# Kernel tuning notes

Measured on AMD Instinct MI355X. Metric: run time of the kernel, lower is better.

Reference implementation:

```python
import jax, jax.numpy as jnp
import numpy as np
from jax import lax
from functools import partial

TAU = 2.0
V_TH = 1.0
ATAN_ALPHA = 2.0
BN_EPS = 1e-5

# Heaviside spike with ATan surrogate gradient (spikingjelly surrogate.ATan, alpha=2)
@jax.custom_vjp
def atan_spike(x):
    return (x >= 0).astype(x.dtype)

def _atan_fwd(x):
    return atan_spike(x), x

def _atan_bwd(x, g):
    # d/dx ~ alpha/2 / (1 + (pi/2 * alpha * x)^2)
    s = (jnp.pi / 2.0) * ATAN_ALPHA * x
    return (g * (ATAN_ALPHA / 2.0) / (1.0 + s * s),)

atan_spike.defvjp(_atan_fwd, _atan_bwd)

def lif_multistep(x_seq):
    # x_seq: [T, B, ...]; LIFNode: decay_input=True, v_reset=0 (hard reset), v0=0
    def step(v, x):
        v = v + (x - v) / TAU           # charge with input decay
        s = atan_spike(v - V_TH)        # fire
        v = v * (1.0 - s)               # hard reset to 0 (reset not detached)
        return v, s
    v0 = jnp.zeros_like(x_seq[0])
    _, s_seq = lax.scan(step, v0, x_seq)
    return s_seq

def conv2d_seq(x_seq, w):
    # x_seq: [T, B, C, H, W] -> flatten T into batch for the conv
    T, B, C, H, W = x_seq.shape
    x = x_seq.reshape(T * B, C, H, W)
    y = lax.conv_general_dilated(x, w, window_strides=(1, 1),
                                 padding=[(1, 1), (1, 1)],
                                 dimension_numbers=('NCHW', 'OIHW', 'NCHW'))
    return y.reshape(T, B, w.shape[0], H, W)

def batchnorm_seq(x_seq, gamma, beta):
    # training-mode BN: stats over merged (T*B, H, W) per channel
    mean = jnp.mean(x_seq, axis=(0, 1, 3, 4), keepdims=True)
    var = jnp.var(x_seq, axis=(0, 1, 3, 4), keepdims=True)
    xhat = (x_seq - mean) * lax.rsqrt(var + BN_EPS)
    return xhat * gamma[None, None, :, None, None] + beta[None, None, :, None, None]

def avgpool2_seq(x_seq):
    T, B, C, H, W = x_seq.shape
    x = x_seq.reshape(T * B, C, H, W)
    y = lax.reduce_window(x, 0.0, lax.add, (1, 1, 2, 2), (1, 1, 2, 2), 'VALID') * 0.25
    return y.reshape(T, B, C, H // 2, W // 2)


def setup_inputs() -> dict:
    key = jax.random.key(0)
    ks = jax.random.split(key, 6)
    T, B = 8, 128
    return {
        'x_seq': jax.random.uniform(ks[0], (T, B, 3, 32, 32), jnp.float32),
        'conv1_w': jax.random.normal(ks[1], (64, 3, 3, 3), jnp.float32) * (1.0 / np.sqrt(3 * 9)),
        'bn1_g': jnp.ones((64,), jnp.float32),
        'bn1_b': jnp.zeros((64,), jnp.float32),
        'conv2_w': jax.random.normal(ks[2], (128, 64, 3, 3), jnp.float32) * (1.0 / np.sqrt(64 * 9)),
        'bn2_g': jnp.ones((128,), jnp.float32),
        'bn2_b': jnp.zeros((128,), jnp.float32),
        'fc1_w': jax.random.normal(ks[3], (256, 8192), jnp.float32) * (1.0 / np.sqrt(8192)),
        'fc2_w': jax.random.normal(ks[4], (10, 256), jnp.float32) * (1.0 / np.sqrt(256)),
        'fc2_b': jnp.zeros((10,), jnp.float32),
    }


def reference(x_seq, conv1_w, bn1_g, bn1_b, conv2_w, bn2_g, bn2_b, fc1_w, fc2_w, fc2_b):
    x = avgpool2_seq(lif_multistep(batchnorm_seq(conv2d_seq(x_seq, conv1_w), bn1_g, bn1_b)))
    x = avgpool2_seq(lif_multistep(batchnorm_seq(conv2d_seq(x, conv2_w), bn2_g, bn2_b)))
    T, B = x.shape[0], x.shape[1]
    x = x.reshape(T, B, -1)                                  # [T, B, 8192]
    x = lif_multistep(jnp.einsum('tbi,oi->tbo', x, fc1_w))   # [T, B, 256]
    logits_seq = jnp.einsum('tbi,oi->tbo', x, fc2_w) + fc2_b # [T, B, 10]
    return logits_seq
```

## Files before the change

kernel.cpp:

```cpp
#include <hip/hip_runtime.h>


#define LIF_STEP(vv, xx, ss) do { \
    vv = fmaf((xx) - vv, 0.5f, vv); \
    ss = (vv >= 1.0f) ? 1.0f : 0.0f; \
    vv = (vv >= 1.0f) ? 0.0f : vv; \
  } while (0)

typedef __attribute__((ext_vector_type(8))) short short8;
typedef __attribute__((ext_vector_type(4))) float f32x4;

__device__ __forceinline__ float bf2f(unsigned short u) {
  return __uint_as_float(((unsigned)u) << 16);
}
__device__ __forceinline__ unsigned short f2bf(float f) {
  return (unsigned short)(__float_as_uint(f) >> 16);
}

#define OFF_POOL1   0u
#define OFF_POOL2   8388608u
#define OFF_PRE     12582912u
#define OFF_STATS   46137344u
#define OFF_FC1S    46162304u
#define OFF_A2      46424448u
#define OFF_B1      46535040u
#define OFF_A1      49680768u
#define ZERO_STATS 24576u

__global__ __launch_bounds__(256) void zero_kernel(float* __restrict__ p, unsigned n) {
  unsigned i = blockIdx.x * 256u + threadIdx.x;
  if (i < n) p[i] = 0.0f;
}

__global__ __launch_bounds__(256) void prep_w1(const float* __restrict__ w, unsigned short* __restrict__ A1) {
  int i = blockIdx.x * 256 + threadIdx.x;
  if (i >= 2048) return;
  int co = i >> 5, k = i & 31;
  float wv = 0.f;
  if (k < 27) {
    int tap = k / 3, ci = k - tap * 3;
    wv = w[co * 27 + ci * 9 + tap];
  }
  unsigned short hi = f2bf(wv);
  float rem = wv - bf2f(hi);
  unsigned short lo = f2bf(rem);
  float rem2 = rem - bf2f(lo);
  A1[i] = hi;
  A1[2048 + i] = lo;
  A1[4096 + i] = f2bf(rem2);
}

__global__ __launch_bounds__(256) void prep_w2(const float* __restrict__ w, unsigned short* __restrict__ A2) {
  int i = blockIdx.x * 256 + threadIdx.x;
  if (i >= 73728) return;
  int co = i / 576, r = i - co * 576;
  int ci = r / 9, t9 = r - ci * 9;
  int k = t9 * 64 + ci;
  int kc = k >> 5, q = (k >> 3) & 3, j = k & 7;
  int off = ((kc * 128 + co) * 4 + q) * 8 + j;
  float wv = w[i];
  unsigned short hi = f2bf(wv);
  float rem = wv - bf2f(hi);
  unsigned short lo = f2bf(rem);
  float rem2 = rem - bf2f(lo);
  A2[off] = hi;
  A2[73728 + off] = lo;
  A2[147456 + off] = f2bf(rem2);
}

__global__ __launch_bounds__(256) void prep_b1(const float* __restrict__ w, unsigned short* __restrict__ B1) {
  __shared__ unsigned short sh[2][8192];
  int blk = blockIdx.x;
  int sv = blk >> 7, opair = blk & 127;
  int tid = threadIdx.x;
  for (int o_l = 0; o_l < 2; ++o_l) {
    for (int it = 0; it < 32; ++it) {
      int korig = tid + 256 * it;
      float wv = w[(size_t)(opair * 2 + o_l) * 8192 + korig];
      unsigned short hi = f2bf(wv);
      float rem = wv - bf2f(hi);
      unsigned short lo = f2bf(rem);
      unsigned short pc = (sv == 0) ? hi : (sv == 1) ? lo : f2bf(rem - bf2f(lo));
      int k = (korig & 63) * 128 + (korig >> 6);
      sh[o_l][k] = pc;
    }
  }
  __syncthreads();
  unsigned short* outp = B1 + (size_t)sv * 2097152;
  for (int it = 0; it < 64; ++it) {
    int idx = tid + 256 * it;
    int kc = idx >> 6, r = idx & 63;
    int o_l = r >> 5, m = r & 31;
    outp[kc * 8192 + opair * 64 + r] = sh[o_l][kc * 32 + m];
  }
}

__global__ void finalize_bn1(const float* __restrict__ s1p,
                             const float* __restrict__ g, const float* __restrict__ b,
                             float* __restrict__ scale, float* __restrict__ shift, float inv_n) {
  int c = threadIdx.x;
  float s1 = 0.f, s2 = 0.f;
#pragma unroll 8
  for (int sp = 0; sp < 64; ++sp) {
    s1 += s1p[sp * 128 + c];
    s2 += s1p[sp * 128 + 64 + c];
  }
  float mean = s1 * inv_n;
  float var = fmaxf(s2 * inv_n - mean * mean, 0.0f);
  float rstd = rsqrtf(var + 1e-5f);
  float sc = g[c] * rstd;
  scale[c] = sc;
  shift[c] = fmaf(-mean, sc, b[c]);
}

__global__ void finalize_bn2(const float* __restrict__ s2p,
                             const float* __restrict__ g, const float* __restrict__ b,
                             float* __restrict__ scale, float* __restrict__ shift, float inv_n) {
  int c = threadIdx.x;
  float s1 = 0.f, s2 = 0.f;
#pragma unroll 8
  for (int sp = 0; sp < 64; ++sp) {
    s1 += s2p[sp * 256 + c];
    s2 += s2p[sp * 256 + 128 + c];
  }
  float mean = s1 * inv_n;
  float var = fmaxf(s2 * inv_n - mean * mean, 0.0f);
  float rstd = rsqrtf(var + 1e-5f);
  float sc = g[c] * rstd;
  scale[c] = sc;
  shift[c] = fmaf(-mean, sc, b[c]);
}

__global__ __launch_bounds__(256) void conv1_pass1_mfma(const float* __restrict__ x,
    const unsigned short* __restrict__ A1, float* __restrict__ s1p) {
  int b = blockIdx.x >> 3, yq = blockIdx.x & 7;
  int y0 = yq * 4;
  int sp = blockIdx.x & 63;
  int tid = threadIdx.x, wave = tid >> 6, lane = tid & 63;
  int xl = lane & 15, q = lane >> 4;
  __shared__ float xs[648];
  short8 A[3][4];
#pragma unroll
  for (int mt = 0; mt < 4; ++mt) {
    int aoff = (mt * 16 + xl) * 32 + q * 8;
    A[0][mt] = *(const short8*)(A1 + aoff);
    A[1][mt] = *(const short8*)(A1 + 2048 + aoff);
    A[2][mt] = *(const short8*)(A1 + 4096 + aoff);
  }
  int cb[8]; bool vld[8];
#pragma unroll
  for (int j = 0; j < 8; ++j) {
    int k = q * 8 + j;
    int tap = k / 3, ci = k - tap * 3;
    int dy = tap / 3, dx = tap - dy * 3;
    vld[j] = (k < 27);
    cb[j] = ci * 216 + (wave + dy) * 36 + dx + xl;
  }
  float s1[4][4], s2[4][4];
#pragma unroll
  for (int mt = 0; mt < 4; ++mt)
#pragma unroll
    for (int reg = 0; reg < 4; ++reg) { s1[mt][reg] = 0.f; s2[mt][reg] = 0.f; }

#pragma unroll 1
  for (int t = 0; t < 8; ++t) {
    int tb = t * 128 + b;
    const float* xb = x + tb * 3072;
    __syncthreads();
    for (int i = tid; i < 648; i += 256) {
      int ci = i / 216, r1 = i - ci * 216;
      int rr = r1 / 36, c = r1 - rr * 36;
      int gy = y0 - 1 + rr, gx = c - 1;
      xs[i] = ((unsigned)gy < 32u && (unsigned)gx < 32u) ? xb[(ci * 32 + gy) * 32 + gx] : 0.f;
    }
    __syncthreads();
    f32x4 acc[2][4];
#pragma unroll
    for (int tile = 0; tile < 2; ++tile)
#pragma unroll
      for (int mt = 0; mt < 4; ++mt) acc[tile][mt] = (f32x4){0.f, 0.f, 0.f, 0.f};
#pragma unroll
    for (int tile = 0; tile < 2; ++tile) {
      short8 Bh = (short8){0,0,0,0,0,0,0,0};
      short8 Bl = (short8){0,0,0,0,0,0,0,0};
      short8 Bll = (short8){0,0,0,0,0,0,0,0};
#pragma unroll
      for (int j = 0; j < 8; ++j) {
        float xv = vld[j] ? xs[cb[j] + tile * 16] : 0.f;
        unsigned short h = f2bf(xv);
        float r = xv - bf2f(h);
        unsigned short l = f2bf(r);
        float r2 = r - bf2f(l);
        Bh[j] = (short)h; Bl[j] = (short)l; Bll[j] = (short)f2bf(r2);
      }
#pragma unroll
      for (int mt = 0; mt < 4; ++mt) {
        f32x4 a = acc[tile][mt];
        a = __builtin_amdgcn_mfma_f32_16x16x32_bf16(A[0][mt], Bh, a, 0, 0, 0);
        a = __builtin_amdgcn_mfma_f32_16x16x32_bf16(A[1][mt], Bh, a, 0, 0, 0);
        a = __builtin_amdgcn_mfma_f32_16x16x32_bf16(A[2][mt], Bh, a, 0, 0, 0);
        a = __builtin_amdgcn_mfma_f32_16x16x32_bf16(A[0][mt], Bl, a, 0, 0, 0);
        a = __builtin_amdgcn_mfma_f32_16x16x32_bf16(A[1][mt], Bl, a, 0, 0, 0);
        a = __builtin_amdgcn_mfma_f32_16x16x32_bf16(A[2][mt], Bl, a, 0, 0, 0);
        a = __builtin_amdgcn_mfma_f32_16x16x32_bf16(A[0][mt], Bll, a, 0, 0, 0);
        a = __builtin_amdgcn_mfma_f32_16x16x32_bf16(A[1][mt], Bll, a, 0, 0, 0);
        acc[tile][mt] = a;
      }
    }
#pragma unroll
    for (int tile = 0; tile < 2; ++tile)
#pragma unroll
      for (int mt = 0; mt < 4; ++mt)
#pragma unroll
        for (int reg = 0; reg < 4; ++reg) {
          float val = acc[tile][mt][reg];
          s1[mt][reg] += val; s2[mt][reg] = fmaf(val, val, s2[mt][reg]);
        }
  }
#pragma unroll
  for (int mt = 0; mt < 4; ++mt)
#pragma unroll
    for (int reg = 0; reg < 4; ++reg) {
      float a1 = s1[mt][reg], a2 = s2[mt][reg];
#pragma unroll
      for (int off = 1; off < 16; off <<= 1) { a1 += __shfl_xor(a1, off); a2 += __shfl_xor(a2, off); }
      if (xl == 0) {
        int co = mt * 16 + q * 4 + reg;
        atomicAdd(&s1p[sp * 128 + co], a1);
        atomicAdd(&s1p[sp * 128 + 64 + co], a2);
      }
    }
}

__global__ __launch_bounds__(256) void conv1_fused_mfma(const float* __restrict__ x,
    const unsigned short* __restrict__ A1, const float* __restrict__ scale,
    const float* __restrict__ shift, unsigned short* __restrict__ pool1) {
  int b = blockIdx.x >> 3, yq = blockIdx.x & 7;
  int y0 = yq * 4;
  int tid = threadIdx.x, wave = tid >> 6, lane = tid & 63;
  int xl = lane & 15, q = lane >> 4;
  __shared__ float xs[648];
  __shared__ unsigned short shout[4 * 16 * 72];
  short8 A[3][4];
#pragma unroll
  for (int mt = 0; mt < 4; ++mt) {
    int aoff = (mt * 16 + xl) * 32 + q * 8;
    A[0][mt] = *(const short8*)(A1 + aoff);
    A[1][mt] = *(const short8*)(A1 + 2048 + aoff);
    A[2][mt] = *(const short8*)(A1 + 4096 + aoff);
  }
  int cb[8]; bool vld[8];
#pragma unroll
  for (int j = 0; j < 8; ++j) {
    int k = q * 8 + j;
    int tap = k / 3, ci = k - tap * 3;
    int dy = tap / 3, dx = tap - dy * 3;
    vld[j] = (k < 27);
    cb[j] = ci * 216 + (wave + dy) * 36 + dx + xl;
  }
  float scr[4][4], shr[4][4];
#pragma unroll
  for (int mt = 0; mt < 4; ++mt)
#pragma unroll
    for (int reg = 0; reg < 4; ++reg) {
      int co = mt * 16 + q * 4 + reg;
      scr[mt][reg] = scale[co]; shr[mt][reg] = shift[co];
    }
  float v[2][4][4];
#pragma unroll
  for (int tile = 0; tile < 2; ++tile)
#pragma unroll
    for (int mt = 0; mt < 4; ++mt)
#pragma unroll
      for (int reg = 0; reg < 4; ++reg) v[tile][mt][reg] = 0.f;

#pragma unroll 1
  for (int t = 0; t < 8; ++t) {
    int tb = t * 128 + b;
    const float* xb = x + tb * 3072;
    __syncthreads();
    for (int i = tid; i < 648; i += 256) {
      int ci = i / 216, r1 = i - ci * 216;
      int rr = r1 / 36, c = r1 - rr * 36;
      int gy = y0 - 1 + rr, gx = c - 1;
      xs[i] = ((unsigned)gy < 32u && (unsigned)gx < 32u) ? xb[(ci * 32 + gy) * 32 + gx] : 0.f;
    }
    __syncthreads();
    f32x4 acc[2][4];
#pragma unroll
    for (int tile = 0; tile < 2; ++tile)
#pragma unroll
      for (int mt = 0; mt < 4; ++mt) acc[tile][mt] = (f32x4){0.f, 0.f, 0.f, 0.f};
#pragma unroll
    for (int tile = 0; tile < 2; ++tile) {
      short8 Bh = (short8){0,0,0,0,0,0,0,0};
      short8 Bl = (short8){0,0,0,0,0,0,0,0};
      short8 Bll = (short8){0,0,0,0,0,0,0,0};
#pragma unroll
      for (int j = 0; j < 8; ++j) {
        float xv = vld[j] ? xs[cb[j] + tile * 16] : 0.f;
        unsigned short h = f2bf(xv);
        float r = xv - bf2f(h);
        unsigned short l = f2bf(r);
        float r2 = r - bf2f(l);
        Bh[j] = (short)h; Bl[j] = (short)l; Bll[j] = (short)f2bf(r2);
      }
#pragma unroll
      for (int mt = 0; mt < 4; ++mt) {
        f32x4 a = acc[tile][mt];
        a = __builtin_amdgcn_mfma_f32_16x16x32_bf16(A[0][mt], Bh, a, 0, 0, 0);
        a = __builtin_amdgcn_mfma_f32_16x16x32_bf16(A[1][mt], Bh, a, 0, 0, 0);
        a = __builtin_amdgcn_mfma_f32_16x16x32_bf16(A[2][mt], Bh, a, 0, 0, 0);
        a = __builtin_amdgcn_mfma_f32_16x16x32_bf16(A[0][mt], Bl, a, 0, 0, 0);
        a = __builtin_amdgcn_mfma_f32_16x16x32_bf16(A[1][mt], Bl, a, 0, 0, 0);
        a = __builtin_amdgcn_mfma_f32_16x16x32_bf16(A[2][mt], Bl, a, 0, 0, 0);
        a = __builtin_amdgcn_mfma_f32_16x16x32_bf16(A[0][mt], Bll, a, 0, 0, 0);
        a = __builtin_amdgcn_mfma_f32_16x16x32_bf16(A[1][mt], Bll, a, 0, 0, 0);
        acc[tile][mt] = a;
      }
    }
#pragma unroll
    for (int mt = 0; mt < 4; ++mt)
#pragma unroll
      for (int rp = 0; rp < 2; ++rp) {
        float hp[2][2];
#pragma unroll
        for (int tile = 0; tile < 2; ++tile)
#pragma unroll
          for (int e = 0; e < 2; ++e) {
            int reg = rp * 2 + e;
            float xv = fmaf(acc[tile][mt][reg], scr[mt][reg], shr[mt][reg]);
            float spk;
            LIF_STEP(v[tile][mt][reg], xv, spk);
            hp[tile][e] = spk + __shfl_xor(spk, 1);
          }
        int tw = xl & 1;
        float h0 = tw ? hp[1][0] : hp[0][0];
        float h1 = tw ? hp[1][1] : hp[0][1];
        unsigned u = (unsigned)f2bf(h0) | ((unsigned)f2bf(h1) << 16);
        int pp = tw * 8 + (xl >> 1);
        *(unsigned*)&shout[(wave * 16 + pp) * 72 + mt * 16 + q * 4 + rp * 2] = u;
      }
    __syncthreads();
    {
      int cg = tid >> 5, py_l = (tid >> 4) & 1, px = tid & 15;
      uint4 ua = *(const uint4*)&shout[((2 * py_l) * 16 + px) * 72 + cg * 8];
      uint4 ub = *(const uint4*)&shout[((2 * py_l + 1) * 16 + px) * 72 + cg * 8];
      const unsigned* pa = (const unsigned*)&ua;
      const unsigned* pb = (const unsigned*)&ub;
      unsigned o[4];
#pragma unroll
      for (int e = 0; e < 4; ++e) {
        float a0 = bf2f((unsigned short)(pa[e] & 0xffffu)), a1 = bf2f((unsigned short)(pa[e] >> 16));
        float b0 = bf2f((unsigned short)(pb[e] & 0xffffu)), b1 = bf2f((unsigned short)(pb[e] >> 16));
        o[e] = (unsigned)f2bf(0.25f * (a0 + b0)) | ((unsigned)f2bf(0.25f * (a1 + b1)) << 16);
      }
      int py = yq * 2 + py_l;
      *(uint4*)(pool1 + (size_t)tb * 16384 + cg * 2048 + (py * 16 + px) * 8) =
          make_uint4(o[0], o[1], o[2], o[3]);
    }
  }
}

__device__ __forceinline__ void c2_load_a(const unsigned short* __restrict__ A2, int kc,
                                          int m0, int xl, int q, short8 (&a)[2][3]) {
#pragma unroll
  for (int mt = 0; mt < 2; ++mt) {
    int aoff = ((kc * 128 + m0 + mt * 16 + xl) * 4 + q) * 8;
    a[mt][0] = *(const short8*)(A2 + aoff);
    a[mt][1] = *(const short8*)(A2 + 73728 + aoff);
    a[mt][2] = *(const short8*)(A2 + 147456 + aoff);
  }
}
__device__ __forceinline__ void c2_step(const unsigned short* __restrict__ simg, int kc,
                                        int xl, int q, short8 (&a)[2][3], f32x4 (&acc)[2][4]) {
  int tap = kc >> 1;
  int dy = tap / 3, dx = tap - dy * 3;
  int cgq = (kc & 1) * 4 + q;
#pragma unroll
  for (int yl = 0; yl < 4; ++yl) {
    int baddr = (((yl + dy) * 8 + cgq) * 18 + (xl + dx)) * 8;
    short8 bb = *(const short8*)(simg + baddr);
#pragma unroll
    for (int mt = 0; mt < 2; ++mt) {
      acc[mt][yl] = __builtin_amdgcn_mfma_f32_16x16x32_bf16(a[mt][0], bb, acc[mt][yl], 0, 0, 0);
      acc[mt][yl] = __builtin_amdgcn_mfma_f32_16x16x32_bf16(a[mt][1], bb, acc[mt][yl], 0, 0, 0);
      acc[mt][yl] = __builtin_amdgcn_mfma_f32_16x16x32_bf16(a[mt][2], bb, acc[mt][yl], 0, 0, 0);
    }
  }
}

__global__ __launch_bounds__(256, 2) void conv2_store_mfma(const unsigned short* __restrict__ pool1,
    const unsigned short* __restrict__ A2, float* __restrict__ preact, float* __restrict__ s2p) {
  int bx = blockIdx.x;
  int tb = bx >> 2, q4 = bx & 3;
  int sp = bx & 63;
  __shared__ unsigned short simg[6 * 8 * 18 * 8];
  int tid = threadIdx.x;
  const unsigned* src = (const unsigned*)(pool1 + (size_t)tb * 16384);
  unsigned* dstw = (unsigned*)simg;
  for (int i = tid; i < 3456; i += 256) {
    int cp = i & 3, rest = i >> 2;
    int jj = rest / 18, xx = rest - jj * 18;
    int cg = jj & 7, row_l = jj >> 3;
    int yi = q4 * 4 - 1 + row_l, gx = xx - 1;
    unsigned val = 0u;
    if ((unsigned)yi < 16u && (unsigned)gx < 16u)
      val = src[cg * 1024 + yi * 64 + gx * 4 + cp];
    dstw[i] = val;
  }
  __syncthreads();

  int wave = tid >> 6, lane = tid & 63;
  int xl = lane & 15, q = lane >> 4;
  int m0 = wave * 32;
  f32x4 acc[2][4];
#pragma unroll
  for (int mt = 0; mt < 2; ++mt)
#pragma unroll
    for (int yl = 0; yl < 4; ++yl) acc[mt][yl] = (f32x4){0.f, 0.f, 0.f, 0.f};

  short8 aA[2][3], aB[2][3];
  c2_load_a(A2, 0, m0, xl, q, aA);
#pragma unroll 1
  for (int kc = 0; kc < 18; kc += 2) {
    c2_load_a(A2, kc + 1, m0, xl, q, aB);
    c2_step(simg, kc, xl, q, aA, acc);
    if (kc + 2 < 18) c2_load_a(A2, kc + 2, m0, xl, q, aA);
    c2_step(simg, kc + 1, xl, q, aB, acc);
  }

  float* pre = preact + (size_t)tb * 32768;
#pragma unroll
  for (int mt = 0; mt < 2; ++mt)
#pragma unroll
    for (int reg = 0; reg < 4; ++reg) {
      int co = m0 + mt * 16 + q * 4 + reg;
      float s1 = 0.f, s2 = 0.f;
#pragma unroll
      for (int yl = 0; yl < 4; ++yl) {
        float val = acc[mt][yl][reg];
        int row = q4 * 4 + yl;
        pre[(row * 128 + co) * 16 + xl] = val;
        s1 += val; s2 = fmaf(val, val, s2);
      }
#pragma unroll
      for (int off = 1; off < 16; off <<= 1) {
        s1 += __shfl_xor(s1, off); s2 += __shfl_xor(s2, off);
      }
      if (xl == 0) {
        atomicAdd(&s2p[sp * 256 + co], s1);
        atomicAdd(&s2p[sp * 256 + 128 + co], s2);
      }
    }
}

__global__ __launch_bounds__(256) void bn2_lif_pool(const float* __restrict__ pre,
    const float* __restrict__ scale, const float* __restrict__ shift,
    unsigned short* __restrict__ pool2) {
  int b = blockIdx.x >> 3, py = blockIdx.x & 7;
  int tid = threadIdx.x;
  int co = tid >> 1, half = tid & 1;
  __shared__ unsigned short shout[8 * 136];
  float sc = scale[co], sh = shift[co];
  float v[4][4];
#pragma unroll
  for (int p = 0; p < 4; ++p)
#pragma unroll
    for (int e = 0; e < 4; ++e) v[p][e] = 0.f;

#pragma unroll 1
  for (int t = 0; t < 8; ++t) {
    const float* base = pre + ((size_t)((t * 128 + b) * 16 + 2 * py)) * 2048 + co * 16 + half * 8;
    __syncthreads();
    float4 r0a = *(const float4*)(base);
    float4 r0b = *(const float4*)(base + 4);
    float4 r1a = *(const float4*)(base + 2048);
    float4 r1b = *(const float4*)(base + 2048 + 4);
    float p00[4] = {r0a.x, r0a.z, r0b.x, r0b.z};
    float p01[4] = {r0a.y, r0a.w, r0b.y, r0b.w};
    float p10[4] = {r1a.x, r1a.z, r1b.x, r1b.z};
    float p11[4] = {r1a.y, r1a.w, r1b.y, r1b.w};
#pragma unroll
    for (int p = 0; p < 4; ++p) {
      float s00, s01, s10, s11, xv;
      xv = fmaf(p00[p], sc, sh); LIF_STEP(v[p][0], xv, s00);
      xv = fmaf(p01[p], sc, sh); LIF_STEP(v[p][1], xv, s01);
      xv = fmaf(p10[p], sc, sh); LIF_STEP(v[p][2], xv, s10);
      xv = fmaf(p11[p], sc, sh); LIF_STEP(v[p][3], xv, s11);
      shout[(half * 4 + p) * 136 + co] = f2bf(0.25f * (s00 + s01 + s10 + s11));
    }
    __syncthreads();
    {
      int s_l = tid >> 5, ci4 = (tid & 31) * 4;
      uint2 vv = *(const uint2*)&shout[s_l * 136 + ci4];
      *(uint2*)(pool2 + ((size_t)(t * 128 + b) * 64 + py * 8 + s_l) * 128 + ci4) = vv;
    }
  }
}

__global__ __launch_bounds__(256, 2) void fc1_mfma(const unsigned short* __restrict__ pool2,
    const unsigned short* __restrict__ B1, float* __restrict__ partial) {
  int bx = blockIdx.x;
  int t_o = bx & 1, tbt = (bx >> 1) & 15, kb = bx >> 5;
  int tid = threadIdx.x, wave = tid >> 6, lane = tid & 63;
  int xl = lane & 15, q = lane >> 4;
  int m0 = t_o * 128 + wave * 32;
  int n0 = tbt * 64;
  __shared__ unsigned short sB[64 * 42];
  f32x4 acc[2][4];
#pragma unroll
  for (int mt = 0; mt < 2; ++mt)
#pragma unroll
    for (int nt = 0; nt < 4; ++nt) acc[mt][nt] = (f32x4){0.f, 0.f, 0.f, 0.f};

#pragma unroll 1
  for (int kc0 = 0; kc0 < 16; ++kc0) {
    int kc = kb * 16 + kc0;
    __syncthreads();
    {
      int tb_l = tid >> 2, kq = tid & 3;
      uint4 vv = *(const uint4*)(pool2 + (size_t)(n0 + tb_l) * 8192 + kc * 32 + kq * 8);
      *(uint4*)(sB + tb_l * 42 + kq * 8) = vv;
    }
    __syncthreads();
    short8 a[2][3];
#pragma unroll
    for (int mt = 0; mt < 2; ++mt) {
      int aoff = ((kc * 256 + m0 + mt * 16 + xl) * 4 + q) * 8;
      a[mt][0] = *(const short8*)(B1 + aoff);
      a[mt][1] = *(const short8*)(B1 + 2097152 + aoff);
      a[mt][2] = *(const short8*)(B1 + 4194304 + aoff);
    }
#pragma unroll
    for (int nt = 0; nt < 4; ++nt) {
      short8 bb = *(const short8*)(sB + (nt * 16 + xl) * 42 + q * 8);
#pragma unroll
      for (int mt = 0; mt < 2; ++mt) {
        acc[mt][nt] = __builtin_amdgcn_mfma_f32_16x16x32_bf16(a[mt][0], bb, acc[mt][nt], 0, 0, 0);
        acc[mt][nt] = __builtin_amdgcn_mfma_f32_16x16x32_bf16(a[mt][1], bb, acc[mt][nt], 0, 0, 0);
        acc[mt][nt] = __builtin_amdgcn_mfma_f32_16x16x32_bf16(a[mt][2], bb, acc[mt][nt], 0, 0, 0);
      }
    }
  }
#pragma unroll
  for (int mt = 0; mt < 2; ++mt)
#pragma unroll
    for (int nt = 0; nt < 4; ++nt)
#pragma unroll
      for (int reg = 0; reg < 4; ++reg) {
        int o = m0 + mt * 16 + q * 4 + reg;
        partial[((size_t)kb * 256 + o) * 1024 + n0 + nt * 16 + xl] = acc[mt][nt][reg];
      }
}

__global__ __launch_bounds__(256) void reduce_lif(const float* __restrict__ partial, float* __restrict__ fs) {
  int idx = blockIdx.x * 256 + threadIdx.x;
  int o = idx >> 7, b = idx & 127;
  float v = 0.f;
#pragma unroll 1
  for (int t = 0; t < 8; ++t) {
    float xv = 0.f;
#pragma unroll
    for (int kb = 0; kb < 16; ++kb)
      xv += partial[((size_t)kb * 256 + o) * 1024 + t * 128 + b];
    float s;
    LIF_STEP(v, xv, s);
    fs[t * 32768 + b * 256 + o] = s;
  }
}

__global__ __launch_bounds__(256) void fc2_kernel(const float* __restrict__ fs, const float* __restrict__ w,
                                                  const float* __restrict__ bias, float* __restrict__ outp) {
  int tb = blockIdx.x;
  __shared__ float sv[256];
  int tid = threadIdx.x;
  sv[tid] = fs[tb * 256 + tid];
  __syncthreads();
  if (tid < 10) {
    float a = bias[tid];
    const float* wr = w + tid * 256;
#pragma unroll 8
    for (int o = 0; o < 256; ++o) a = fmaf(sv[o], wr[o], a);
    outp[tb * 10 + tid] = a;
  }
}

extern "C" void kernel_launch(void* const* d_in, const int* in_sizes, int n_in,
                              void* d_out, int out_size, void* d_ws, size_t ws_size,
                              hipStream_t stream) {
  (void)in_sizes; (void)n_in; (void)out_size; (void)ws_size;
  const float* x_seq   = (const float*)d_in[0];
  const float* conv1_w = (const float*)d_in[1];
  const float* bn1_g   = (const float*)d_in[2];
  const float* bn1_b   = (const float*)d_in[3];
  const float* conv2_w = (const float*)d_in[4];
  const float* bn2_g   = (const float*)d_in[5];
  const float* bn2_b   = (const float*)d_in[6];
  const float* fc1_w   = (const float*)d_in[7];
  const float* fc2_w   = (const float*)d_in[8];
  const float* fc2_b   = (const float*)d_in[9];
  float* out = (float*)d_out;
  float* ws  = (float*)d_ws;

  unsigned short* pool1 = (unsigned short*)(ws + OFF_POOL1);
  float* fc1_part = ws + OFF_POOL1;
  unsigned short* pool2 = (unsigned short*)(ws + OFF_POOL2);
  float* preact  = ws + OFF_PRE;
  float* fc1_s   = ws + OFF_FC1S;
  unsigned short* A2 = (unsigned short*)(ws + OFF_A2);
  unsigned short* B1 = (unsigned short*)(ws + OFF_B1);
  unsigned short* A1 = (unsigned short*)(ws + OFF_A1);
  float* st      = ws + OFF_STATS;
  float* s1p    = st;
  float* s2p    = st + 8192;
  float* bn1_sc = st + 24576;  float* bn1_sh = st + 24640;
  float* bn2_sc = st + 24704;  float* bn2_sh = st + 24832;

  zero_kernel<<<96, 256, 0, stream>>>(st, ZERO_STATS);
  prep_w1<<<8, 256, 0, stream>>>(conv1_w, A1);
  prep_w2<<<288, 256, 0, stream>>>(conv2_w, A2);
  prep_b1<<<384, 256, 0, stream>>>(fc1_w, B1);
  conv1_pass1_mfma<<<1024, 256, 0, stream>>>(x_seq, A1, s1p);
  finalize_bn1<<<1, 64, 0, stream>>>(s1p, bn1_g, bn1_b, bn1_sc, bn1_sh, 1.0f / 1048576.0f);
  conv1_fused_mfma<<<1024, 256, 0, stream>>>(x_seq, A1, bn1_sc, bn1_sh, pool1);
  conv2_store_mfma<<<4096, 256, 0, stream>>>(pool1, A2, preact, s2p);
  finalize_bn2<<<1, 128, 0, stream>>>(s2p, bn2_g, bn2_b, bn2_sc, bn2_sh, 1.0f / 262144.0f);
  bn2_lif_pool<<<1024, 256, 0, stream>>>(preact, bn2_sc, bn2_sh, pool2);
  fc1_mfma<<<512, 256, 0, stream>>>(pool2, B1, fc1_part);
  reduce_lif<<<128, 256, 0, stream>>>(fc1_part, fc1_s);
  fc2_kernel<<<1024, 256, 0, stream>>>(fc1_s, fc2_w, fc2_b, out);
}
```

Before: 402.5 us.

## Enlarge conv2 spatial tile to 8 rows and halve fc1 barrier count

Each conv2 block now computes 8 output rows instead of 4, so each loaded A2 weight fragment feeds twice as many MFMAs and the halo overhead in shared memory drops. The grid is halved to 2048 blocks and the accumulators double to 64 floats per lane, which adds register pressure under the 2-blocks-per-SM launch bound. Separately, fc1 stages two K-chunks per barrier pair into a double-sized shared buffer, halving the number of __syncthreads.

```diff
diff --git a/kernel.cpp b/kernel.cpp
--- a/kernel.cpp
+++ b/kernel.cpp
@@ -372,13 +372,13 @@
     a[mt][2] = *(const short8*)(A2 + 147456 + aoff);
   }
 }
-__device__ __forceinline__ void c2_step(const unsigned short* __restrict__ simg, int kc,
-                                        int xl, int q, short8 (&a)[2][3], f32x4 (&acc)[2][4]) {
+__device__ __forceinline__ void c2_step8(const unsigned short* __restrict__ simg, int kc,
+                                         int xl, int q, short8 (&a)[2][3], f32x4 (&acc)[2][8]) {
   int tap = kc >> 1;
   int dy = tap / 3, dx = tap - dy * 3;
   int cgq = (kc & 1) * 4 + q;
 #pragma unroll
-  for (int yl = 0; yl < 4; ++yl) {
+  for (int yl = 0; yl < 8; ++yl) {
     int baddr = (((yl + dy) * 8 + cgq) * 18 + (xl + dx)) * 8;
     short8 bb = *(const short8*)(simg + baddr);
 #pragma unroll
@@ -393,17 +393,17 @@
 __global__ __launch_bounds__(256, 2) void conv2_store_mfma(const unsigned short* __restrict__ pool1,
     const unsigned short* __restrict__ A2, float* __restrict__ preact, float* __restrict__ s2p) {
   int bx = blockIdx.x;
-  int tb = bx >> 2, q4 = bx & 3;
+  int tb = bx >> 1, half = bx & 1;
   int sp = bx & 63;
-  __shared__ unsigned short simg[6 * 8 * 18 * 8];
+  __shared__ unsigned short simg[10 * 8 * 18 * 8];
   int tid = threadIdx.x;
   const unsigned* src = (const unsigned*)(pool1 + (size_t)tb * 16384);
   unsigned* dstw = (unsigned*)simg;
-  for (int i = tid; i < 3456; i += 256) {
+  for (int i = tid; i < 5760; i += 256) {
     int cp = i & 3, rest = i >> 2;
     int jj = rest / 18, xx = rest - jj * 18;
     int cg = jj & 7, row_l = jj >> 3;
-    int yi = q4 * 4 - 1 + row_l, gx = xx - 1;
+    int yi = half * 8 - 1 + row_l, gx = xx - 1;
     unsigned val = 0u;
     if ((unsigned)yi < 16u && (unsigned)gx < 16u)
       val = src[cg * 1024 + yi * 64 + gx * 4 + cp];
@@ -414,20 +414,20 @@
   int wave = tid >> 6, lane = tid & 63;
   int xl = lane & 15, q = lane >> 4;
   int m0 = wave * 32;
-  f32x4 acc[2][4];
+  f32x4 acc[2][8];
 #pragma unroll
   for (int mt = 0; mt < 2; ++mt)
 #pragma unroll
-    for (int yl = 0; yl < 4; ++yl) acc[mt][yl] = (f32x4){0.f, 0.f, 0.f, 0.f};
+    for (int yl = 0; yl < 8; ++yl) acc[mt][yl] = (f32x4){0.f, 0.f, 0.f, 0.f};
 
   short8 aA[2][3], aB[2][3];
   c2_load_a(A2, 0, m0, xl, q, aA);
 #pragma unroll 1
   for (int kc = 0; kc < 18; kc += 2) {
     c2_load_a(A2, kc + 1, m0, xl, q, aB);
-    c2_step(simg, kc, xl, q, aA, acc);
+    c2_step8(simg, kc, xl, q, aA, acc);
     if (kc + 2 < 18) c2_load_a(A2, kc + 2, m0, xl, q, aA);
-    c2_step(simg, kc + 1, xl, q, aB, acc);
+    c2_step8(simg, kc + 1, xl, q, aB, acc);
   }
 
   float* pre = preact + (size_t)tb * 32768;
@@ -438,9 +438,9 @@
       int co = m0 + mt * 16 + q * 4 + reg;
       float s1 = 0.f, s2 = 0.f;
 #pragma unroll
-      for (int yl = 0; yl < 4; ++yl) {
+      for (int yl = 0; yl < 8; ++yl) {
         float val = acc[mt][yl][reg];
-        int row = q4 * 4 + yl;
+        int row = half * 8 + yl;
         pre[(row * 128 + co) * 16 + xl] = val;
         s1 += val; s2 = fmaf(val, val, s2);
       }
@@ -507,7 +507,7 @@
   int xl = lane & 15, q = lane >> 4;
   int m0 = t_o * 128 + wave * 32;
   int n0 = tbt * 64;
-  __shared__ unsigned short sB[64 * 42];
+  __shared__ unsigned short sB[2][64 * 42];
   f32x4 acc[2][4];
 #pragma unroll
   for (int mt = 0; mt < 2; ++mt)
@@ -515,31 +515,38 @@
     for (int nt = 0; nt < 4; ++nt) acc[mt][nt] = (f32x4){0.f, 0.f, 0.f, 0.f};
 
 #pragma unroll 1
-  for (int kc0 = 0; kc0 < 16; ++kc0) {
+  for (int kc0 = 0; kc0 < 16; kc0 += 2) {
     int kc = kb * 16 + kc0;
     __syncthreads();
     {
       int tb_l = tid >> 2, kq = tid & 3;
-      uint4 vv = *(const uint4*)(pool2 + (size_t)(n0 + tb_l) * 8192 + kc * 32 + kq * 8);
-      *(uint4*)(sB + tb_l * 42 + kq * 8) = vv;
-    }
-    __syncthreads();
-    short8 a[2][3];
-#pragma unroll
-    for (int mt = 0; mt < 2; ++mt) {
-      int aoff = ((kc * 256 + m0 + mt * 16 + xl) * 4 + q) * 8;
-      a[mt][0] = *(const short8*)(B1 + aoff);
-      a[mt][1] = *(const short8*)(B1 + 2097152 + aoff);
-      a[mt][2] = *(const short8*)(B1 + 4194304 + aoff);
-    }
-#pragma unroll
-    for (int nt = 0; nt < 4; ++nt) {
-      short8 bb = *(const short8*)(sB + (nt * 16 + xl) * 42 + q * 8);
+      const unsigned short* srcp = pool2 + (size_t)(n0 + tb_l) * 8192 + kc * 32 + kq * 8;
+      uint4 v0 = *(const uint4*)(srcp);
+      uint4 v1 = *(const uint4*)(srcp + 32);
+      *(uint4*)(sB[0] + tb_l * 42 + kq * 8) = v0;
+      *(uint4*)(sB[1] + tb_l * 42 + kq * 8) = v1;
+    }
+    __syncthreads();
+#pragma unroll
+    for (int sub = 0; sub < 2; ++sub) {
+      int kcs = kc + sub;
+      short8 a[2][3];
 #pragma unroll
       for (int mt = 0; mt < 2; ++mt) {
-        acc[mt][nt] = __builtin_amdgcn_mfma_f32_16x16x32_bf16(a[mt][0], bb, acc[mt][nt], 0, 0, 0);
-        acc[mt][nt] = __builtin_amdgcn_mfma_f32_16x16x32_bf16(a[mt][1], bb, acc[mt][nt], 0, 0, 0);
-        acc[mt][nt] = __builtin_amdgcn_mfma_f32_16x16x32_bf16(a[mt][2], bb, acc[mt][nt], 0, 0, 0);
+        int aoff = ((kcs * 256 + m0 + mt * 16 + xl) * 4 + q) * 8;
+        a[mt][0] = *(const short8*)(B1 + aoff);
+        a[mt][1] = *(const short8*)(B1 + 2097152 + aoff);
+        a[mt][2] = *(const short8*)(B1 + 4194304 + aoff);
+      }
+#pragma unroll
+      for (int nt = 0; nt < 4; ++nt) {
+        short8 bb = *(const short8*)(sB[sub] + (nt * 16 + xl) * 42 + q * 8);
+#pragma unroll
+        for (int mt = 0; mt < 2; ++mt) {
+          acc[mt][nt] = __builtin_amdgcn_mfma_f32_16x16x32_bf16(a[mt][0], bb, acc[mt][nt], 0, 0, 0);
+          acc[mt][nt] = __builtin_amdgcn_mfma_f32_16x16x32_bf16(a[mt][1], bb, acc[mt][nt], 0, 0, 0);
+          acc[mt][nt] = __builtin_amdgcn_mfma_f32_16x16x32_bf16(a[mt][2], bb, acc[mt][nt], 0, 0, 0);
+        }
       }
     }
   }
@@ -624,7 +631,7 @@
   conv1_pass1_mfma<<<1024, 256, 0, stream>>>(x_seq, A1, s1p);
   finalize_bn1<<<1, 64, 0, stream>>>(s1p, bn1_g, bn1_b, bn1_sc, bn1_sh, 1.0f / 1048576.0f);
   conv1_fused_mfma<<<1024, 256, 0, stream>>>(x_seq, A1, bn1_sc, bn1_sh, pool1);
-  conv2_store_mfma<<<4096, 256, 0, stream>>>(pool1, A2, preact, s2p);
+  conv2_store_mfma<<<2048, 256, 0, stream>>>(pool1, A2, preact, s2p);
   finalize_bn2<<<1, 128, 0, stream>>>(s2p, bn2_g, bn2_b, bn2_sc, bn2_sh, 1.0f / 262144.0f);
   bn2_lif_pool<<<1024, 256, 0, stream>>>(preact, bn2_sc, bn2_sh, pool2);
   fc1_mfma<<<512, 256, 0, stream>>>(pool2, B1, fc1_part);
```

Measured after the change: 362.7 us. 1.11x faster.
